# Kernel optimization log

Measured on AMD Instinct MI355X. Metric: run time of the kernel, lower is better.

## Reference

```python
import jax, jax.numpy as jnp
import numpy as np

B, TGT, SRC, SRC_DIM, TGT_DIM = 4, 4096, 4096, 256, 256
NEG_BIG = 1.0e11   # additive mask constant from the torch code
CLAMP_MIN = -1.0e10


def setup_inputs() -> dict:
    key = jax.random.key(0)
    k1, k2, k3, k4 = jax.random.split(key, 4)
    h_t = jax.random.normal(k1, (B, TGT, TGT_DIM), dtype=jnp.float32)
    h_s = jax.random.normal(k2, (B, SRC, SRC_DIM), dtype=jnp.float32)
    m_s = jax.random.randint(k3, (B, SRC), 0, 2, dtype=jnp.int32)
    # linear_in: nn.Linear(src_dim, tgt_dim, bias=False) -> weight [tgt_dim, src_dim]
    lim = float(np.sqrt(1.0 / SRC_DIM))
    W_in = jax.random.uniform(k4, (TGT_DIM, SRC_DIM), dtype=jnp.float32, minval=-lim, maxval=lim)
    return {"h_t": h_t, "h_s": h_s, "m_s": m_s, "W_in": W_in}


def reference(h_t, h_s, m_s, W_in):
    # 'general' score: h_t @ (linear_in(h_s))^T
    energy = jnp.einsum("bsd,td->bst", h_s, W_in)          # (B, S, tgt_dim)
    scores = jnp.einsum("btd,bsd->bts", h_t, energy)        # (B, T, S)
    m = m_s.astype(scores.dtype)[:, None, :]                 # (B, 1, S)
    scores = scores * m - NEG_BIG * (1.0 - m)
    scores = jax.nn.softmax(jnp.maximum(scores, CLAMP_MIN), axis=-1)
    context = jnp.einsum("bts,bsd->btd", scores, h_s)        # (B, T, src_dim)
    return context, scores
```

## Files before the change

### kernel.cpp

```cpp
#include <hip/hip_runtime.h>
#include <cstdint>
#include <cstddef>

typedef _Float16 f16;
typedef _Float16 half8 __attribute__((ext_vector_type(8)));
typedef float floatx4 __attribute__((ext_vector_type(4)));
typedef unsigned short ushort8 __attribute__((ext_vector_type(8)));

__device__ __forceinline__ void gload_lds16(const void* g, void* l) {
    __builtin_amdgcn_global_load_lds(
        (const __attribute__((address_space(1))) void*)g,
        (__attribute__((address_space(3))) void*)l,
        16, 0, 0);
}

__device__ __forceinline__ unsigned short f32_to_bf16(float f) {
    unsigned u = __float_as_uint(f);
    return (unsigned short)((u + 0x7FFFu + ((u >> 16) & 1u)) >> 16);
}
__device__ __forceinline__ float bf16_to_f32(unsigned short h) {
    return __uint_as_float(((unsigned)h) << 16);
}

__global__ void k_cvt2(const float* __restrict__ srcA, f16* __restrict__ dstA, int n8a,
                       const float* __restrict__ srcB, f16* __restrict__ dstB, int n8b) {
    int i = blockIdx.x * blockDim.x + threadIdx.x;
    const float* src;
    f16* dst;
    int j;
    if (i < n8a) { src = srcA; dst = dstA; j = i; }
    else { j = i - n8a; if (j >= n8b) return; src = srcB; dst = dstB; }
    const float4* s = (const float4*)src + 2 * (size_t)j;
    float4 a = s[0], b = s[1];
    half8 h;
    h[0] = (f16)a.x; h[1] = (f16)a.y; h[2] = (f16)a.z; h[3] = (f16)a.w;
    h[4] = (f16)b.x; h[5] = (f16)b.y; h[6] = (f16)b.z; h[7] = (f16)b.w;
    ((half8*)dst)[j] = h;
}

__global__ void k_hs(const float* __restrict__ hs, f16* __restrict__ hs16, f16* __restrict__ hsT) {
    int id = blockIdx.x;
    int dt = id & 3;
    int st = (id >> 2) & 63;
    int b  = id >> 8;
    __shared__ f16 tile[64][65];
    int t = threadIdx.x;
    int s0 = st * 64, d0 = dt * 64;
#pragma unroll
    for (int i = 0; i < 16; i++) {
        int e = t + i * 256;
        int r = e >> 6, c = e & 63;
        float v = hs[((size_t)(b * 4096 + s0 + r)) * 256 + d0 + c];
        f16 hv = (f16)v;
        hs16[((size_t)(b * 4096 + s0 + r)) * 256 + d0 + c] = hv;
        tile[r][c] = hv;
    }
    __syncthreads();
#pragma unroll
    for (int i = 0; i < 16; i++) {
        int e = t + i * 256;
        int r = e >> 6, c = e & 63;
        hsT[((size_t)(b * 256 + d0 + r)) * 4096 + s0 + c] = tile[c][r];
    }
}

__global__ __launch_bounds__(256, 2) void k_energy(
    const f16* __restrict__ A,
    const f16* __restrict__ Bt,
    f16* __restrict__ C)
{
    int id = blockIdx.x;
    int tn = id & 1, tm = (id >> 1) & 31, b = id >> 6;
    const f16* Ab = A + (size_t)b * 4096 * 256;

    __shared__ __align__(16) f16 As[128 * 64];
    __shared__ __align__(16) f16 Bs[128 * 64];

    int tid = threadIdx.x;
    int wave = tid >> 6, lane = tid & 63;
    int wr = wave >> 1, wc = wave & 1;
    int lm = lane & 15, lq = lane >> 4;

    floatx4 acc[4][4] = {};
    int r0 = tm * 128, c0 = tn * 128;

    for (int k0 = 0; k0 < 256; k0 += 64) {
#pragma unroll
        for (int i = 0; i < 4; i++) {
            int rbase = wave * 32 + i * 8;
            int row = rbase + (lane >> 3);
            gload_lds16(Ab + (size_t)(r0 + row) * 256 + k0 + (lane & 7) * 8, &As[rbase * 64]);
            gload_lds16(Bt + (size_t)(c0 + row) * 256 + k0 + (lane & 7) * 8, &Bs[rbase * 64]);
        }
        __syncthreads();
        half8 af[4][2], bf[4][2];
#pragma unroll
        for (int mi = 0; mi < 4; mi++)
#pragma unroll
            for (int kk = 0; kk < 2; kk++) {
                af[mi][kk] = *(const half8*)&As[(wr * 64 + mi * 16 + lm) * 64 + kk * 32 + lq * 8];
                bf[mi][kk] = *(const half8*)&Bs[(wc * 64 + mi * 16 + lm) * 64 + kk * 32 + lq * 8];
            }
#pragma unroll
        for (int kk = 0; kk < 2; kk++)
#pragma unroll
            for (int mi = 0; mi < 4; mi++)
#pragma unroll
                for (int ni = 0; ni < 4; ni++)
                    acc[mi][ni] = __builtin_amdgcn_mfma_f32_16x16x32_f16(af[mi][kk], bf[ni][kk], acc[mi][ni], 0, 0, 0);
        __syncthreads();
    }
#pragma unroll
    for (int mi = 0; mi < 4; mi++)
#pragma unroll
        for (int ni = 0; ni < 4; ni++)
#pragma unroll
            for (int r = 0; r < 4; r++) {
                int row = r0 + wr * 64 + mi * 16 + lq * 4 + r;
                int col = c0 + wc * 64 + ni * 16 + lm;
                C[(size_t)(b * 4096 + row) * 256 + col] = (f16)acc[mi][ni][r];
            }
}

__global__ __launch_bounds__(256, 2) void k_scores(
    const f16* __restrict__ A,
    const f16* __restrict__ Bt,
    const int* __restrict__ ms,
    unsigned short* __restrict__ E,
    float* __restrict__ rsum)
{
    int id = blockIdx.x;
    int tn = id & 31, tm = (id >> 5) & 31, b = id >> 10;
    const f16* Ab = A + (size_t)b * 4096 * 256;
    const f16* Bb = Bt + (size_t)b * 4096 * 256;

    __shared__ __align__(16) f16 As[128 * 64];
    __shared__ __align__(16) f16 Bs[128 * 64];

    int tid = threadIdx.x;
    int wave = tid >> 6, lane = tid & 63;
    int wr = wave >> 1, wc = wave & 1;
    int lm = lane & 15, lq = lane >> 4;

    floatx4 acc[4][4] = {};
    int r0 = tm * 128, c0 = tn * 128;

    for (int k0 = 0; k0 < 256; k0 += 64) {
#pragma unroll
        for (int i = 0; i < 4; i++) {
            int rbase = wave * 32 + i * 8;
            int row = rbase + (lane >> 3);
            gload_lds16(Ab + (size_t)(r0 + row) * 256 + k0 + (lane & 7) * 8, &As[rbase * 64]);
            gload_lds16(Bb + (size_t)(c0 + row) * 256 + k0 + (lane & 7) * 8, &Bs[rbase * 64]);
        }
        __syncthreads();
        half8 af[4][2], bf[4][2];
#pragma unroll
        for (int mi = 0; mi < 4; mi++)
#pragma unroll
            for (int kk = 0; kk < 2; kk++) {
                af[mi][kk] = *(const half8*)&As[(wr * 64 + mi * 16 + lm) * 64 + kk * 32 + lq * 8];
                bf[mi][kk] = *(const half8*)&Bs[(wc * 64 + mi * 16 + lm) * 64 + kk * 32 + lq * 8];
            }
#pragma unroll
        for (int kk = 0; kk < 2; kk++)
#pragma unroll
            for (int mi = 0; mi < 4; mi++)
#pragma unroll
                for (int ni = 0; ni < 4; ni++)
                    acc[mi][ni] = __builtin_amdgcn_mfma_f32_16x16x32_f16(af[mi][kk], bf[ni][kk], acc[mi][ni], 0, 0, 0);
        __syncthreads();
    }
    float rs[4][4] = {};
#pragma unroll
    for (int ni = 0; ni < 4; ni++) {
        int col = c0 + wc * 64 + ni * 16 + lm;
        int m = ms[b * 4096 + col];
#pragma unroll
        for (int mi = 0; mi < 4; mi++)
#pragma unroll
            for (int r = 0; r < 4; r++) {
                int row = r0 + wr * 64 + mi * 16 + lq * 4 + r;
                float e = m ? __expf(acc[mi][ni][r]) : 0.0f;
                E[(size_t)(b * 4096 + row) * 4096 + col] = f32_to_bf16(e);
                rs[mi][r] += e;
            }
    }
#pragma unroll
    for (int mi = 0; mi < 4; mi++)
#pragma unroll
        for (int r = 0; r < 4; r++) {
            float v = rs[mi][r];
#pragma unroll
            for (int off = 1; off < 16; off <<= 1)
                v += __shfl_xor(v, off, 16);
            if (lm == 0) {
                int row = r0 + wr * 64 + mi * 16 + lq * 4 + r;
                atomicAdd(&rsum[b * 4096 + row], v);
            }
        }
}

__global__ __launch_bounds__(512, 4) void k_ctx(
    const f16* __restrict__ BtT,
    const unsigned short* __restrict__ E,
    float* __restrict__ P,
    const float* __restrict__ rsum,
    f16* __restrict__ part)
{
    int id = blockIdx.x;
    int ks = id & 3, tt = (id >> 2) & 31, b = id >> 7;
    int tid = threadIdx.x;
    int wave = tid >> 6, lane = tid & 63;
    int lm = lane & 15, lq = lane >> 4;

    __shared__ __align__(16) f16 Bs0[8 * 2048];
    __shared__ __align__(16) f16 Bs1[8 * 2048];

    int t0 = tt * 128;
    const f16* Bb = BtT + (size_t)b * 256 * 4096;

    int row = t0 + wave * 16 + lm;
    int gr = b * 4096 + row;
    float rinv = 1.0f / rsum[gr];
    size_t rowbase = (size_t)gr * 4096;

    int g = wave;
    int cg = 2 * (g & 3);
    const f16* gp = Bb + (size_t)(lane ^ cg) * 4096 + g * 8;
    int lds_off = g * 2048;

    int rbk[2];
    rbk[0] = (0 * 4 + lq) * 2048 + (lm ^ (2 * lq)) * 8;
    rbk[1] = (1 * 4 + lq) * 2048 + (lm ^ (2 * lq)) * 8;

    floatx4 acc[16] = {};
    int sbeg = ks * 1024;

#pragma unroll
    for (int R = 0; R < 256; R += 64) {
        gload_lds16(gp + (size_t)R * 4096 + sbeg, &Bs0[lds_off + R * 8]);
    }
    __syncthreads();

#define CTX_ITER(IT, BSR, BSW) do { \
    int s0c_ = sbeg + (IT) * 64; \
    ushort8 ev_[2]; \
    _Pragma("unroll") \
    for (int kk = 0; kk < 2; kk++) \
        ev_[kk] = *(const ushort8*)(E + rowbase + s0c_ + kk * 32 + lq * 8); \
    if ((IT) < 15) { \
        int s0n_ = s0c_ + 64; \
        _Pragma("unroll") \
        for (int R = 0; R < 256; R += 64) { \
            gload_lds16(gp + (size_t)R * 4096 + s0n_, &BSW[lds_off + R * 8]); \
        } \
    } \
    half8 af_[2]; \
    _Pragma("unroll") \
    for (int kk = 0; kk < 2; kk++) { \
        half8 h_; \
        _Pragma("unroll") \
        for (int j = 0; j < 8; j++) \
            h_[j] = (f16)(bf16_to_f32(ev_[kk][j]) * rinv); \
        af_[kk] = h_; \
    } \
    _Pragma("unroll") \
    for (int kk = 0; kk < 2; kk++) { \
        float* p_ = P + rowbase + s0c_ + kk * 32 + lq * 8; \
        half8 h_ = af_[kk]; \
        ((float4*)p_)[0] = make_float4((float)h_[0], (float)h_[1], (float)h_[2], (float)h_[3]); \
        ((float4*)p_)[1] = make_float4((float)h_[4], (float)h_[5], (float)h_[6], (float)h_[7]); \
    } \
    _Pragma("unroll") \
    for (int kk = 0; kk < 2; kk++) \
        _Pragma("unroll") \
        for (int ni = 0; ni < 16; ni++) { \
            half8 bf_ = *(const half8*)&BSR[rbk[kk] + ni * 128]; \
            acc[ni] = __builtin_amdgcn_mfma_f32_16x16x32_f16(af_[kk], bf_, acc[ni], 0, 0, 0); \
        } \
    __syncthreads(); \
    } while (0)

    for (int it = 0; it < 16; it += 2) {
        CTX_ITER(it, Bs0, Bs1);
        CTX_ITER(it + 1, Bs1, Bs0);
    }
#undef CTX_ITER

    f16* Pp = part + (size_t)ks * 4194304 + (size_t)b * 1048576;
#pragma unroll
    for (int ni = 0; ni < 16; ni++)
#pragma unroll
        for (int r = 0; r < 4; r++) {
            int orow = t0 + wave * 16 + lq * 4 + r;
            int col = ni * 16 + lm;
            Pp[(size_t)orow * 256 + col] = (f16)acc[ni][r];
        }
}

__global__ void k_red(const f16* __restrict__ part, float* __restrict__ out) {
    size_t i = (size_t)blockIdx.x * 256 + threadIdx.x;
    const half8* p = (const half8*)part;
    half8 a = p[i];
    half8 b = p[i + 524288];
    half8 c = p[i + 1048576];
    half8 d = p[i + 1572864];
    float4 o0, o1;
    o0.x = (float)a[0] + (float)b[0] + (float)c[0] + (float)d[0];
    o0.y = (float)a[1] + (float)b[1] + (float)c[1] + (float)d[1];
    o0.z = (float)a[2] + (float)b[2] + (float)c[2] + (float)d[2];
    o0.w = (float)a[3] + (float)b[3] + (float)c[3] + (float)d[3];
    o1.x = (float)a[4] + (float)b[4] + (float)c[4] + (float)d[4];
    o1.y = (float)a[5] + (float)b[5] + (float)c[5] + (float)d[5];
    o1.z = (float)a[6] + (float)b[6] + (float)c[6] + (float)d[6];
    o1.w = (float)a[7] + (float)b[7] + (float)c[7] + (float)d[7];
    ((float4*)out)[2 * i] = o0;
    ((float4*)out)[2 * i + 1] = o1;
}

extern "C" void kernel_launch(void* const* d_in, const int* in_sizes, int n_in,
                              void* d_out, int out_size, void* d_ws, size_t ws_size,
                              hipStream_t stream) {
    const float* h_t = (const float*)d_in[0];
    const float* h_s = (const float*)d_in[1];
    const int*   m_s = (const int*)d_in[2];
    const float* W   = (const float*)d_in[3];

    float* out = (float*)d_out;
    char* ws = (char*)d_ws;
    f16* h_t16 = (f16*)(ws);
    f16* h_s16 = (f16*)(ws + 8388608);
    f16* h_sT  = (f16*)(ws + 16777216);
    f16* en16  = (f16*)(ws + 25165824);
    f16* W16   = (f16*)(ws + 33554432);
    float* rsum = (float*)(ws + 33685504);
    unsigned short* e16 = (unsigned short*)(ws + 33751040);
    f16* part = (f16*)(ws + 167968768);

    float* ctx = out;
    float* sc  = out + 4194304;

    hipMemsetAsync(rsum, 0, 16384 * sizeof(float), stream);
    k_cvt2<<<2080, 256, 0, stream>>>(h_t, h_t16, 524288, W, W16, 8192);
    k_hs<<<1024, 256, 0, stream>>>(h_s, h_s16, h_sT);
    k_energy<<<256, 256, 0, stream>>>(h_s16, W16, en16);
    k_scores<<<4096, 256, 0, stream>>>(h_t16, en16, m_s, e16, rsum);
    k_ctx<<<512, 512, 0, stream>>>(h_sT, e16, sc, rsum, part);
    k_red<<<2048, 256, 0, stream>>>(part, ctx);
}
```

Measured before the change: 503.6 us.

## Double-buffer scores GEMM LDS tiles and prefetch E rows in context kernel

The scores kernel's K loop is unrolled with two LDS buffer pairs, so the global-to-LDS load of the next K slice is issued before the MFMAs on the current slice, hiding load latency. LDS use per block doubles to 64 KB, which may limit occupancy at the requested two blocks per CU. In the context kernel, the bf16 exp values for the next 64-column chunk are loaded one iteration early into registers, overlapping their global latency with the current MFMAs at the cost of extra VGPRs.

```diff
diff --git a/kernel.cpp b/kernel.cpp
--- a/kernel.cpp
+++ b/kernel.cpp
@@ -122,6 +122,33 @@
             }
 }
 
+#define GE_STAGE(AS, BS, K0) do { \
+    _Pragma("unroll") \
+    for (int i_ = 0; i_ < 4; i_++) { \
+        int rbase_ = wave * 32 + i_ * 8; \
+        int row_ = rbase_ + (lane >> 3); \
+        gload_lds16(Ab + (size_t)(r0 + row_) * 256 + (K0) + (lane & 7) * 8, &AS[rbase_ * 64]); \
+        gload_lds16(Bsrc + (size_t)(c0 + row_) * 256 + (K0) + (lane & 7) * 8, &BS[rbase_ * 64]); \
+    } } while (0)
+
+#define GE_COMPUTE(AS, BS) do { \
+    half8 af_[4][2], bf_[4][2]; \
+    _Pragma("unroll") \
+    for (int mi_ = 0; mi_ < 4; mi_++) \
+        _Pragma("unroll") \
+        for (int kk_ = 0; kk_ < 2; kk_++) { \
+            af_[mi_][kk_] = *(const half8*)&AS[(wr * 64 + mi_ * 16 + lm) * 64 + kk_ * 32 + lq * 8]; \
+            bf_[mi_][kk_] = *(const half8*)&BS[(wc * 64 + mi_ * 16 + lm) * 64 + kk_ * 32 + lq * 8]; \
+        } \
+    _Pragma("unroll") \
+    for (int kk_ = 0; kk_ < 2; kk_++) \
+        _Pragma("unroll") \
+        for (int mi_ = 0; mi_ < 4; mi_++) \
+            _Pragma("unroll") \
+            for (int ni_ = 0; ni_ < 4; ni_++) \
+                acc[mi_][ni_] = __builtin_amdgcn_mfma_f32_16x16x32_f16(af_[mi_][kk_], bf_[ni_][kk_], acc[mi_][ni_], 0, 0, 0); \
+    } while (0)
+
 __global__ __launch_bounds__(256, 2) void k_scores(
     const f16* __restrict__ A,
     const f16* __restrict__ Bt,
@@ -132,10 +159,12 @@
     int id = blockIdx.x;
     int tn = id & 31, tm = (id >> 5) & 31, b = id >> 10;
     const f16* Ab = A + (size_t)b * 4096 * 256;
-    const f16* Bb = Bt + (size_t)b * 4096 * 256;
-
-    __shared__ __align__(16) f16 As[128 * 64];
-    __shared__ __align__(16) f16 Bs[128 * 64];
+    const f16* Bsrc = Bt + (size_t)b * 4096 * 256;
+
+    __shared__ __align__(16) f16 As0[128 * 64];
+    __shared__ __align__(16) f16 Bs0[128 * 64];
+    __shared__ __align__(16) f16 As1[128 * 64];
+    __shared__ __align__(16) f16 Bs1[128 * 64];
 
     int tid = threadIdx.x;
     int wave = tid >> 6, lane = tid & 63;
@@ -145,32 +174,19 @@
     floatx4 acc[4][4] = {};
     int r0 = tm * 128, c0 = tn * 128;
 
-    for (int k0 = 0; k0 < 256; k0 += 64) {
-#pragma unroll
-        for (int i = 0; i < 4; i++) {
-            int rbase = wave * 32 + i * 8;
-            int row = rbase + (lane >> 3);
-            gload_lds16(Ab + (size_t)(r0 + row) * 256 + k0 + (lane & 7) * 8, &As[rbase * 64]);
-            gload_lds16(Bb + (size_t)(c0 + row) * 256 + k0 + (lane & 7) * 8, &Bs[rbase * 64]);
-        }
-        __syncthreads();
-        half8 af[4][2], bf[4][2];
-#pragma unroll
-        for (int mi = 0; mi < 4; mi++)
-#pragma unroll
-            for (int kk = 0; kk < 2; kk++) {
-                af[mi][kk] = *(const half8*)&As[(wr * 64 + mi * 16 + lm) * 64 + kk * 32 + lq * 8];
-                bf[mi][kk] = *(const half8*)&Bs[(wc * 64 + mi * 16 + lm) * 64 + kk * 32 + lq * 8];
-            }
-#pragma unroll
-        for (int kk = 0; kk < 2; kk++)
-#pragma unroll
-            for (int mi = 0; mi < 4; mi++)
-#pragma unroll
-                for (int ni = 0; ni < 4; ni++)
-                    acc[mi][ni] = __builtin_amdgcn_mfma_f32_16x16x32_f16(af[mi][kk], bf[ni][kk], acc[mi][ni], 0, 0, 0);
-        __syncthreads();
-    }
+    GE_STAGE(As0, Bs0, 0);
+    __syncthreads();
+    GE_STAGE(As1, Bs1, 64);
+    GE_COMPUTE(As0, Bs0);
+    __syncthreads();
+    GE_STAGE(As0, Bs0, 128);
+    GE_COMPUTE(As1, Bs1);
+    __syncthreads();
+    GE_STAGE(As1, Bs1, 192);
+    GE_COMPUTE(As0, Bs0);
+    __syncthreads();
+    GE_COMPUTE(As1, Bs1);
+
     float rs[4][4] = {};
 #pragma unroll
     for (int ni = 0; ni < 4; ni++) {
@@ -237,6 +253,9 @@
     floatx4 acc[16] = {};
     int sbeg = ks * 1024;
 
+    ushort8 ev[2];
+    ev[0] = *(const ushort8*)(E + rowbase + sbeg + 0 * 32 + lq * 8);
+    ev[1] = *(const ushort8*)(E + rowbase + sbeg + 1 * 32 + lq * 8);
 #pragma unroll
     for (int R = 0; R < 256; R += 64) {
         gload_lds16(gp + (size_t)R * 4096 + sbeg, &Bs0[lds_off + R * 8]);
@@ -244,25 +263,24 @@
     __syncthreads();
 
 #define CTX_ITER(IT, BSR, BSW) do { \
-    int s0c_ = sbeg + (IT) * 64; \
-    ushort8 ev_[2]; \
-    _Pragma("unroll") \
-    for (int kk = 0; kk < 2; kk++) \
-        ev_[kk] = *(const ushort8*)(E + rowbase + s0c_ + kk * 32 + lq * 8); \
+    ushort8 evn_[2]; \
     if ((IT) < 15) { \
-        int s0n_ = s0c_ + 64; \
+        int s0n_ = sbeg + ((IT) + 1) * 64; \
+        evn_[0] = *(const ushort8*)(E + rowbase + s0n_ + 0 * 32 + lq * 8); \
+        evn_[1] = *(const ushort8*)(E + rowbase + s0n_ + 1 * 32 + lq * 8); \
         _Pragma("unroll") \
         for (int R = 0; R < 256; R += 64) { \
             gload_lds16(gp + (size_t)R * 4096 + s0n_, &BSW[lds_off + R * 8]); \
         } \
     } \
+    int s0c_ = sbeg + (IT) * 64; \
     half8 af_[2]; \
     _Pragma("unroll") \
     for (int kk = 0; kk < 2; kk++) { \
         half8 h_; \
         _Pragma("unroll") \
         for (int j = 0; j < 8; j++) \
-            h_[j] = (f16)(bf16_to_f32(ev_[kk][j]) * rinv); \
+            h_[j] = (f16)(bf16_to_f32(ev[kk][j]) * rinv); \
         af_[kk] = h_; \
     } \
     _Pragma("unroll") \
@@ -280,6 +298,7 @@
             acc[ni] = __builtin_amdgcn_mfma_f32_16x16x32_f16(af_[kk], bf_, acc[ni], 0, 0, 0); \
         } \
     __syncthreads(); \
+    if ((IT) < 15) { ev[0] = evn_[0]; ev[1] = evn_[1]; } \
     } while (0)
 
     for (int it = 0; it < 16; it += 2) {
```

After: 528.2 us. 4.9% more time.
